# Kernel optimization log

Hardware: AMD Instinct MI355X
Metric: run time of the kernel (lower is better)

## Reference

```python
import jax, jax.numpy as jnp
import numpy as np

H, QK, VD = 16, 64, 64  # n_heads, qk_dim, v_dim

def _feature_map(t):
    # elu(x) + 1, the standard positive feature map for linear attention
    return jax.nn.elu(t) + 1.0

def setup_inputs() -> dict:
    key = jax.random.key(0)
    ks = jax.random.split(key, 5)
    B, T, D = 2, 4096, 1024
    s = 0.02
    return {
        "x": jax.random.normal(ks[0], (B, T, D), dtype=jnp.float32),
        "WQ": jax.random.normal(ks[1], (H * QK, D), dtype=jnp.float32) * s,
        "WK": jax.random.normal(ks[2], (H * QK, D), dtype=jnp.float32) * s,
        "WV": jax.random.normal(ks[3], (H * VD, D), dtype=jnp.float32) * s,
        "Wproj": jax.random.normal(ks[4], (D, VD), dtype=jnp.float32) * s,
        "start_pos": 0,
    }

def reference(x, WQ, WK, WV, Wproj, start_pos):
    B, T, D = x.shape
    # QKV projections (no bias), reshape to heads
    q = (x @ WQ.T).reshape(B, T, H, QK)
    k = (x @ WK.T).reshape(B, T, H, QK)
    v = (x @ WV.T).reshape(B, T, H, VD)
    q = _feature_map(q)
    k = _feature_map(k)
    # global key-value summary per head: [B,H,QK,VD]
    kv = jnp.einsum('bthd,bthm->bhdm', k, v)
    # normalizer: q . sum_t(k)
    z = 1.0 / jnp.einsum('bthd,bhd->bth', q, k.sum(axis=1))
    o = jnp.einsum('bthd,bhdm->bthm', q, kv) * z[..., None]  # [B,T,H,VD]
    # per-head output projection (module applies Linear(v_dim, dim) on last axis)
    return jnp.einsum('bthm,cm->bthc', o, Wproj)  # [B,T,H,D]
```

## Files before the change

kernel.cpp:

```cpp
#include <hip/hip_runtime.h>

#define Bb 2
#define Tt 4096
#define Dd 1024
#define Hh 16
#define QKd 64
#define VDd 64
#define BT (Bb*Tt)
#define NCH 16
#define CHUNK (Tt/NCH)

#define OFF_QF  0
#define OFF_KF  (OFF_QF + (size_t)BT*Dd)
#define OFF_V   (OFF_KF + (size_t)BT*512)
#define OFF_KVP (OFF_V + (size_t)BT*512)
#define OFF_KSP (OFF_KVP + (size_t)NCH*32*4096)
#define OFF_KV  (OFF_KSP + (size_t)NCH*32*64)
#define OFF_KS  (OFF_KV + (size_t)32*4096)
#define OFF_XA  (OFF_KS + (size_t)32*64)
#define OFF_WB  (OFF_XA + (size_t)BT*512)
#define OFF_KVQB (OFF_WB + (size_t)3072*512)
#define OFF_QSB (OFF_KVQB + (size_t)32*1024*32)

typedef __attribute__((ext_vector_type(8))) short short8;
typedef __attribute__((ext_vector_type(4))) float f32x4;

__device__ __forceinline__ float featmap(float x) {
    return x > 0.f ? x + 1.f : __expf(x);
}

__device__ __forceinline__ unsigned short bf16_rne(float f) {
    unsigned int u = __float_as_uint(f);
    unsigned int r = u + 0x7fffu + ((u >> 16) & 1u);
    return (unsigned short)(r >> 16);
}
__device__ __forceinline__ float bf16_to_f(unsigned short h) {
    return __uint_as_float(((unsigned int)h) << 16);
}

__global__ __launch_bounds__(256) void cast_a(const float* __restrict__ src,
                                              unsigned short* __restrict__ dst)
{
    int idx = blockIdx.x * 256 + threadIdx.x;
    int m = idx >> 8;
    int c = (idx & 255) << 2;
    float4 v = *(const float4*)&src[(size_t)m * 1024 + c];
    ushort4 o;
    o.x = bf16_rne(v.x); o.y = bf16_rne(v.y); o.z = bf16_rne(v.z); o.w = bf16_rne(v.w);
    *(ushort4*)&dst[(size_t)m * 1024 + c] = o;
}

__global__ __launch_bounds__(256) void cast_w3(const float* __restrict__ WQ,
                                               const float* __restrict__ WK,
                                               const float* __restrict__ WV,
                                               unsigned short* __restrict__ dst)
{
    int idx = blockIdx.x * 256 + threadIdx.x;
    int w = idx >> 18;
    int r = idx & 262143;
    const float* src = (w == 0) ? WQ : ((w == 1) ? WK : WV);
    int m = r >> 8;
    int c = (r & 255) << 2;
    float4 v = *(const float4*)&src[(size_t)m * 1024 + c];
    ushort4 o;
    o.x = bf16_rne(v.x); o.y = bf16_rne(v.y); o.z = bf16_rne(v.z); o.w = bf16_rne(v.w);
    *(ushort4*)&dst[(size_t)(w*1024 + m) * 1024 + c] = o;
}

#define GLLDS(gp, lp) __builtin_amdgcn_global_load_lds( \
    (const __attribute__((address_space(1))) void*)(gp), \
    (__attribute__((address_space(3))) void*)(lp), 16, 0, 0)

__global__ __launch_bounds__(512, 2) void gemm_qkv(const unsigned short* __restrict__ A,
                                                   const unsigned short* __restrict__ W,
                                                   float* __restrict__ qf,
                                                   unsigned short* __restrict__ kfb,
                                                   unsigned short* __restrict__ vfb)
{
    extern __shared__ unsigned short lds[];
    const int tid  = threadIdx.x;
    const int lane = tid & 63;
    const int wave = tid >> 6;
    const int wm = (wave >> 2) * 128;
    const int wn = (wave & 3) * 64;
    const int bid = blockIdx.x;
    const int nb = (bid & 7) * 48 + (bid >> 3);
    const int mblk = nb / 12, nblk = nb % 12;
    const int m0 = mblk * 256, n0 = nblk * 256;

    f32x4 acc[8][4] = {};

    auto stage = [&](int buf, int kt) {
        const int k0 = kt * 64;
        unsigned short* ab = &lds[buf * 32768];
        unsigned short* bb = ab + 16384;
        #pragma unroll
        for (int i = 0; i < 4; ++i) {
            int s = i * 512 + tid;
            int row = s >> 3, g = s & 7;
            int gl = g ^ (row & 7);
            GLLDS(&A[(size_t)(m0 + row) * 1024 + k0 + gl * 8], &ab[s * 8]);
        }
        #pragma unroll
        for (int i = 0; i < 4; ++i) {
            int s = i * 512 + tid;
            int row = s >> 3, g = s & 7;
            int gl = g ^ (row & 7);
            GLLDS(&W[(size_t)(n0 + row) * 1024 + k0 + gl * 8], &bb[s * 8]);
        }
    };

    stage(0, 0);
    for (int kt = 0; kt < 16; ++kt) {
        const int buf = kt & 1;
        if (kt + 1 < 16) {
            stage(buf ^ 1, kt + 1);
            asm volatile("s_waitcnt vmcnt(8)" ::: "memory");
        } else {
            asm volatile("s_waitcnt vmcnt(0)" ::: "memory");
        }
        __builtin_amdgcn_s_barrier();
        __builtin_amdgcn_sched_barrier(0);
        const unsigned short* ab = &lds[buf * 32768];
        const unsigned short* bb = ab + 16384;
        #pragma unroll
        for (int ks = 0; ks < 2; ++ks) {
            short8 af[8], bf2[4];
            #pragma unroll
            for (int mi = 0; mi < 8; ++mi) {
                int row = wm + mi * 16 + (lane & 15);
                int g = ks * 4 + (lane >> 4);
                af[mi] = *(const short8*)&ab[row * 64 + (g ^ (row & 7)) * 8];
            }
            #pragma unroll
            for (int ni = 0; ni < 4; ++ni) {
                int row = wn + ni * 16 + (lane & 15);
                int g = ks * 4 + (lane >> 4);
                bf2[ni] = *(const short8*)&bb[row * 64 + (g ^ (row & 7)) * 8];
            }
            __builtin_amdgcn_s_setprio(1);
            #pragma unroll
            for (int mi = 0; mi < 8; ++mi)
                #pragma unroll
                for (int ni = 0; ni < 4; ++ni)
                    acc[mi][ni] = __builtin_amdgcn_mfma_f32_16x16x32_bf16(af[mi], bf2[ni], acc[mi][ni], 0, 0, 0);
            __builtin_amdgcn_s_setprio(0);
        }
        __builtin_amdgcn_s_barrier();
        __builtin_amdgcn_sched_barrier(0);
    }

    const int c0 = n0 & 1023;
    if (n0 < 1024) {
        #pragma unroll
        for (int mi = 0; mi < 8; ++mi)
            #pragma unroll
            for (int ni = 0; ni < 4; ++ni)
                #pragma unroll
                for (int r = 0; r < 4; ++r) {
                    int row = m0 + wm + mi*16 + ((lane >> 4) << 2) + r;
                    int col = c0 + wn + ni*16 + (lane & 15);
                    qf[(size_t)row * 1024 + col] = featmap(acc[mi][ni][r]);
                }
    } else if (n0 < 2048) {
        #pragma unroll
        for (int mi = 0; mi < 8; ++mi)
            #pragma unroll
            for (int ni = 0; ni < 4; ++ni)
                #pragma unroll
                for (int r = 0; r < 4; ++r) {
                    int row = m0 + wm + mi*16 + ((lane >> 4) << 2) + r;
                    int col = c0 + wn + ni*16 + (lane & 15);
                    kfb[(size_t)row * 1024 + col] = bf16_rne(featmap(acc[mi][ni][r]));
                }
    } else {
        #pragma unroll
        for (int mi = 0; mi < 8; ++mi)
            #pragma unroll
            for (int ni = 0; ni < 4; ++ni)
                #pragma unroll
                for (int r = 0; r < 4; ++r) {
                    int row = m0 + wm + mi*16 + ((lane >> 4) << 2) + r;
                    int col = c0 + wn + ni*16 + (lane & 15);
                    vfb[(size_t)row * 1024 + col] = bf16_rne(acc[mi][ni][r]);
                }
    }
}

__global__ __launch_bounds__(256) void kv_partial(const unsigned short* __restrict__ kfb,
        const unsigned short* __restrict__ vfb, float* __restrict__ kvpart,
        float* __restrict__ kspart)
{
    const int bh = blockIdx.x;
    const int ch = blockIdx.y;
    const int b = bh >> 4, h = bh & 15;
    __shared__ float sk[8][64];
    __shared__ float sv[8][64];
    const int tid = threadIdx.x;
    const int r0 = (tid >> 4) << 2;
    const int c0 = (tid & 15) << 2;
    const int tt = tid >> 5;
    const int rem = tid & 31;
    const int which = rem >> 4;
    const int d4 = (rem & 15) << 2;
    const unsigned short* src = which ? vfb : kfb;
    float acc[4][4] = {};
    float ksl = 0.f;
    for (int t0 = ch * CHUNK; t0 < (ch + 1) * CHUNK; t0 += 8) {
        const int t = t0 + tt;
        ushort4 val = *(const ushort4*)&src[(size_t)(b*Tt + t)*Dd + h*QKd + d4];
        float4 f;
        f.x = bf16_to_f(val.x); f.y = bf16_to_f(val.y);
        f.z = bf16_to_f(val.z); f.w = bf16_to_f(val.w);
        __syncthreads();
        if (which) *(float4*)&sv[tt][d4] = f;
        else       *(float4*)&sk[tt][d4] = f;
        __syncthreads();
        #pragma unroll
        for (int s = 0; s < 8; ++s) {
            float4 k4v = *(const float4*)&sk[s][r0];
            float4 v4v = *(const float4*)&sv[s][c0];
            float kvv[4] = {k4v.x,k4v.y,k4v.z,k4v.w};
            float vvv[4] = {v4v.x,v4v.y,v4v.z,v4v.w};
            #pragma unroll
            for (int i = 0; i < 4; ++i)
                #pragma unroll
                for (int j = 0; j < 4; ++j)
                    acc[i][j] = fmaf(kvv[i], vvv[j], acc[i][j]);
        }
        if (tid < 64) {
            #pragma unroll
            for (int s = 0; s < 8; ++s) ksl += sk[s][tid];
        }
    }
    const size_t base = (size_t)(ch*32 + bh) * 4096;
    #pragma unroll
    for (int i = 0; i < 4; ++i) {
        float4 o = {acc[i][0], acc[i][1], acc[i][2], acc[i][3]};
        *(float4*)&kvpart[base + (r0+i)*64 + c0] = o;
    }
    if (tid < 64) kspart[(size_t)(ch*32 + bh)*64 + tid] = ksl;
}

__global__ __launch_bounds__(256) void kv_reduce(const float* __restrict__ kvpart,
        const float* __restrict__ kspart, float* __restrict__ kv, float* __restrict__ ksum)
{
    int g = blockIdx.x * 256 + threadIdx.x;
    if (g < 32*4096) {
        float s = 0.f;
        #pragma unroll
        for (int c = 0; c < NCH; ++c) s += kvpart[(size_t)c*(32*4096) + g];
        kv[g] = s;
    } else if (g < 32*4096 + 32*64) {
        int g2 = g - 32*4096;
        float s = 0.f;
        #pragma unroll
        for (int c = 0; c < NCH; ++c) s += kspart[(size_t)c*(32*64) + g2];
        ksum[g2] = s;
    }
}

__global__ __launch_bounds__(256) void kvpb_kernel(const float* __restrict__ kv,
        const float* __restrict__ wproj, unsigned short* __restrict__ kvqb)
{
    int flat = blockIdx.x * 256 + threadIdx.x;
    int d = flat & 63;
    int c = (flat >> 6) & 1023;
    int bh = flat >> 16;
    const float4* kr = (const float4*)&kv[(size_t)(bh*64 + d)*64];
    const float4* wr = (const float4*)&wproj[(size_t)c*64];
    float s = 0.f;
    #pragma unroll
    for (int m = 0; m < 16; ++m) {
        float4 a = kr[m], bq = wr[m];
        s += a.x*bq.x + a.y*bq.y + a.z*bq.z + a.w*bq.w;
    }
    kvqb[((size_t)bh*1024 + c) * 64 + d] = bf16_rne(s);
}

__global__ __launch_bounds__(256) void zq_kernel(const float* __restrict__ qf,
        const float* __restrict__ ksum, unsigned short* __restrict__ qsb)
{
    int row = blockIdx.x * 16 + (threadIdx.x >> 4);
    int l16 = threadIdx.x & 15;
    int bt = row >> 4, h = row & 15;
    int b = bt >> 12, t = bt & 4095;
    float4 qv = *(const float4*)&qf[(size_t)bt*1024 + h*64 + l16*4];
    float4 kq = *(const float4*)&ksum[(size_t)(b*16 + h)*64 + l16*4];
    float p = qv.x*kq.x + qv.y*kq.y + qv.z*kq.z + qv.w*kq.w;
    p += __shfl_xor(p, 1); p += __shfl_xor(p, 2);
    p += __shfl_xor(p, 4); p += __shfl_xor(p, 8);
    float zv = 1.f / p;
    ushort4 o;
    o.x = bf16_rne(qv.x*zv); o.y = bf16_rne(qv.y*zv);
    o.z = bf16_rne(qv.z*zv); o.w = bf16_rne(qv.w*zv);
    *(ushort4*)&qsb[(((size_t)(b*16 + h)*4096 + t) << 6) + l16*4] = o;
}

__global__ __launch_bounds__(256) void fgemm(const unsigned short* __restrict__ qsb,
        const unsigned short* __restrict__ kvqb, float* __restrict__ out)
{
    __shared__ unsigned short Als[2][128*32];
    __shared__ unsigned short Bls[2][128*32];
    const int tid  = threadIdx.x;
    const int lane = tid & 63;
    const int wave = tid >> 6;
    const int bh = blockIdx.z;
    const int b = bh >> 4, h = bh & 15;
    const int t0 = blockIdx.y * 128;
    const int c0 = blockIdx.x * 128;
    const int wr = (wave >> 1) * 64;
    const int wc = (wave & 1) * 64;
    f32x4 acc[4][4] = {};

    auto stage = [&](int buf, int kt) {
        const int k0 = kt * 32;
        #pragma unroll
        for (int i = 0; i < 2; ++i) {
            int s = i * 256 + tid;
            int row = s >> 2, g = s & 3;
            GLLDS(&qsb[((size_t)bh*4096 + t0 + row) * 64 + k0 + g * 8], &Als[buf][s * 8]);
            GLLDS(&kvqb[((size_t)bh*1024 + c0 + row) * 64 + k0 + g * 8], &Bls[buf][s * 8]);
        }
    };

    stage(0, 0);
    const int arow = (lane & 15) * 32 + (lane >> 4) * 8;
    for (int kt = 0; kt < 2; ++kt) {
        const int buf = kt & 1;
        __syncthreads();
        if (kt + 1 < 2) stage(buf ^ 1, kt + 1);
        short8 af[4], bfr[4];
        #pragma unroll
        for (int m = 0; m < 4; ++m)
            af[m] = *(const short8*)&Als[buf][(wr + m*16)*32 + arow];
        #pragma unroll
        for (int n = 0; n < 4; ++n)
            bfr[n] = *(const short8*)&Bls[buf][(wc + n*16)*32 + arow];
        #pragma unroll
        for (int m = 0; m < 4; ++m)
            #pragma unroll
            for (int n = 0; n < 4; ++n)
                acc[m][n] = __builtin_amdgcn_mfma_f32_16x16x32_bf16(af[m], bfr[n], acc[m][n], 0, 0, 0);
    }

    #pragma unroll
    for (int m = 0; m < 4; ++m) {
        #pragma unroll
        for (int n = 0; n < 4; ++n) {
            #pragma unroll
            for (int r = 0; r < 4; ++r) {
                int trow = t0 + wr + m*16 + ((lane >> 4) << 2) + r;
                int col = c0 + wc + n*16 + (lane & 15);
                out[((size_t)(b*4096 + trow)*16 + h)*1024 + col] = acc[m][n][r];
            }
        }
    }
}

extern "C" void kernel_launch(void* const* d_in, const int* in_sizes, int n_in,
                              void* d_out, int out_size, void* d_ws, size_t ws_size,
                              hipStream_t stream)
{
    const float* x  = (const float*)d_in[0];
    const float* WQ = (const float*)d_in[1];
    const float* WK = (const float*)d_in[2];
    const float* WV = (const float*)d_in[3];
    const float* Wp = (const float*)d_in[4];
    float* ws = (float*)d_ws;
    float* qf     = ws + OFF_QF;
    unsigned short* kfb = (unsigned short*)(ws + OFF_KF);
    unsigned short* vfb = (unsigned short*)(ws + OFF_V);
    float* kvpart = ws + OFF_KVP;
    float* kspart = ws + OFF_KSP;
    float* kv     = ws + OFF_KV;
    float* ksum   = ws + OFF_KS;
    unsigned short* xa   = (unsigned short*)(ws + OFF_XA);
    unsigned short* wb   = (unsigned short*)(ws + OFF_WB);
    unsigned short* kvqb = (unsigned short*)(ws + OFF_KVQB);
    unsigned short* qsb  = (unsigned short*)(ws + OFF_QSB);
    float* out = (float*)d_out;

    (void)hipFuncSetAttribute((const void*)gemm_qkv,
                              hipFuncAttributeMaxDynamicSharedMemorySize, 131072);

    dim3 blk(256);
    cast_a<<<(BT*1024/4)/256, blk, 0, stream>>>(x, xa);
    cast_w3<<<(3*1024*1024/4)/256, blk, 0, stream>>>(WQ, WK, WV, wb);
    gemm_qkv<<<384, 512, 131072, stream>>>(xa, wb, qf, kfb, vfb);
    kv_partial<<<dim3(32, NCH), blk, 0, stream>>>(kfb, vfb, kvpart, kspart);
    kv_reduce<<<(32*4096 + 32*64 + 255)/256, blk, 0, stream>>>(kvpart, kspart, kv, ksum);
    kvpb_kernel<<<(32*1024*64)/256, blk, 0, stream>>>(kv, Wp, kvqb);
    zq_kernel<<<(BT*Hh)/16, blk, 0, stream>>>(qf, ksum, qsb);
    fgemm<<<dim3(8, 32, 32), blk, 0, stream>>>(qsb, kvqb, out);
}
```

Before: 315.6 us.

## Merge cast kernels and restage kv_partial with larger time tiles

Fuses the two bf16 cast kernels into one launch, removing one kernel launch and its tail. Restructures kv_partial to stage 32 timesteps per iteration with padded LDS rows and wider per-thread loads, cutting the number of barriers per chunk. Halves the number of time chunks, which gives fewer blocks (256) but longer per-block loops and less partial-reduction data. The lower chunk count may reduce parallelism in kv_partial.

```diff
diff --git a/kernel.cpp b/kernel.cpp
--- a/kernel.cpp
+++ b/kernel.cpp
@@ -7,7 +7,7 @@
 #define QKd 64
 #define VDd 64
 #define BT (Bb*Tt)
-#define NCH 16
+#define NCH 8
 #define CHUNK (Tt/NCH)
 
 #define OFF_QF  0
@@ -38,33 +38,33 @@
     return __uint_as_float(((unsigned int)h) << 16);
 }
 
-__global__ __launch_bounds__(256) void cast_a(const float* __restrict__ src,
-                                              unsigned short* __restrict__ dst)
+__global__ __launch_bounds__(256) void cast_all(const float* __restrict__ x,
+                                                const float* __restrict__ WQ,
+                                                const float* __restrict__ WK,
+                                                const float* __restrict__ WV,
+                                                unsigned short* __restrict__ xa,
+                                                unsigned short* __restrict__ wbuf)
 {
     int idx = blockIdx.x * 256 + threadIdx.x;
-    int m = idx >> 8;
-    int c = (idx & 255) << 2;
-    float4 v = *(const float4*)&src[(size_t)m * 1024 + c];
-    ushort4 o;
-    o.x = bf16_rne(v.x); o.y = bf16_rne(v.y); o.z = bf16_rne(v.z); o.w = bf16_rne(v.w);
-    *(ushort4*)&dst[(size_t)m * 1024 + c] = o;
-}
-
-__global__ __launch_bounds__(256) void cast_w3(const float* __restrict__ WQ,
-                                               const float* __restrict__ WK,
-                                               const float* __restrict__ WV,
-                                               unsigned short* __restrict__ dst)
-{
-    int idx = blockIdx.x * 256 + threadIdx.x;
-    int w = idx >> 18;
-    int r = idx & 262143;
-    const float* src = (w == 0) ? WQ : ((w == 1) ? WK : WV);
-    int m = r >> 8;
-    int c = (r & 255) << 2;
-    float4 v = *(const float4*)&src[(size_t)m * 1024 + c];
-    ushort4 o;
-    o.x = bf16_rne(v.x); o.y = bf16_rne(v.y); o.z = bf16_rne(v.z); o.w = bf16_rne(v.w);
-    *(ushort4*)&dst[(size_t)(w*1024 + m) * 1024 + c] = o;
+    if (idx < 2097152) {
+        int m = idx >> 8;
+        int c = (idx & 255) << 2;
+        float4 v = *(const float4*)&x[(size_t)m * 1024 + c];
+        ushort4 o;
+        o.x = bf16_rne(v.x); o.y = bf16_rne(v.y); o.z = bf16_rne(v.z); o.w = bf16_rne(v.w);
+        *(ushort4*)&xa[(size_t)m * 1024 + c] = o;
+    } else {
+        int r = idx - 2097152;
+        int w = r >> 18;
+        int rr = r & 262143;
+        const float* src = (w == 0) ? WQ : ((w == 1) ? WK : WV);
+        int m = rr >> 8;
+        int c = (rr & 255) << 2;
+        float4 v = *(const float4*)&src[(size_t)m * 1024 + c];
+        ushort4 o;
+        o.x = bf16_rne(v.x); o.y = bf16_rne(v.y); o.z = bf16_rne(v.z); o.w = bf16_rne(v.w);
+        *(ushort4*)&wbuf[(size_t)(w*1024 + m) * 1024 + c] = o;
+    }
 }
 
 #define GLLDS(gp, lp) __builtin_amdgcn_global_load_lds( \
@@ -194,30 +194,37 @@
     const int bh = blockIdx.x;
     const int ch = blockIdx.y;
     const int b = bh >> 4, h = bh & 15;
-    __shared__ float sk[8][64];
-    __shared__ float sv[8][64];
+    __shared__ float sk[32][68];
+    __shared__ float sv[32][68];
     const int tid = threadIdx.x;
     const int r0 = (tid >> 4) << 2;
     const int c0 = (tid & 15) << 2;
-    const int tt = tid >> 5;
-    const int rem = tid & 31;
-    const int which = rem >> 4;
-    const int d4 = (rem & 15) << 2;
+    const int which = tid >> 7;
+    const int rr = (tid & 127) >> 2;
+    const int d16 = (tid & 3) << 4;
     const unsigned short* src = which ? vfb : kfb;
     float acc[4][4] = {};
     float ksl = 0.f;
-    for (int t0 = ch * CHUNK; t0 < (ch + 1) * CHUNK; t0 += 8) {
-        const int t = t0 + tt;
-        ushort4 val = *(const ushort4*)&src[(size_t)(b*Tt + t)*Dd + h*QKd + d4];
-        float4 f;
-        f.x = bf16_to_f(val.x); f.y = bf16_to_f(val.y);
-        f.z = bf16_to_f(val.z); f.w = bf16_to_f(val.w);
+    for (int t0 = ch * CHUNK; t0 < (ch + 1) * CHUNK; t0 += 32) {
+        const int t = t0 + rr;
+        const unsigned short* sp = &src[(size_t)(b*Tt + t)*Dd + h*QKd + d16];
+        ushort4 ua = *(const ushort4*)&sp[0];
+        ushort4 ub = *(const ushort4*)&sp[4];
+        ushort4 uc = *(const ushort4*)&sp[8];
+        ushort4 ud = *(const ushort4*)&sp[12];
+        float4 f0 = {bf16_to_f(ua.x), bf16_to_f(ua.y), bf16_to_f(ua.z), bf16_to_f(ua.w)};
+        float4 f1 = {bf16_to_f(ub.x), bf16_to_f(ub.y), bf16_to_f(ub.z), bf16_to_f(ub.w)};
+        float4 f2 = {bf16_to_f(uc.x), bf16_to_f(uc.y), bf16_to_f(uc.z), bf16_to_f(uc.w)};
+        float4 f3 = {bf16_to_f(ud.x), bf16_to_f(ud.y), bf16_to_f(ud.z), bf16_to_f(ud.w)};
         __syncthreads();
-        if (which) *(float4*)&sv[tt][d4] = f;
-        else       *(float4*)&sk[tt][d4] = f;
+        float* dst = which ? &sv[rr][d16] : &sk[rr][d16];
+        *(float4*)&dst[0]  = f0;
+        *(float4*)&dst[4]  = f1;
+        *(float4*)&dst[8]  = f2;
+        *(float4*)&dst[12] = f3;
         __syncthreads();
-        #pragma unroll
-        for (int s = 0; s < 8; ++s) {
+        #pragma unroll 8
+        for (int s = 0; s < 32; ++s) {
             float4 k4v = *(const float4*)&sk[s][r0];
             float4 v4v = *(const float4*)&sv[s][c0];
             float kvv[4] = {k4v.x,k4v.y,k4v.z,k4v.w};
@@ -229,8 +236,8 @@
                     acc[i][j] = fmaf(kvv[i], vvv[j], acc[i][j]);
         }
         if (tid < 64) {
-            #pragma unroll
-            for (int s = 0; s < 8; ++s) ksl += sk[s][tid];
+            #pragma unroll 8
+            for (int s = 0; s < 32; ++s) ksl += sk[s][tid];
         }
     }
     const size_t base = (size_t)(ch*32 + bh) * 4096;
@@ -385,8 +392,7 @@
                               hipFuncAttributeMaxDynamicSharedMemorySize, 131072);
 
     dim3 blk(256);
-    cast_a<<<(BT*1024/4)/256, blk, 0, stream>>>(x, xa);
-    cast_w3<<<(3*1024*1024/4)/256, blk, 0, stream>>>(WQ, WK, WV, wb);
+    cast_all<<<(2097152 + 786432)/256, blk, 0, stream>>>(x, WQ, WK, WV, xa, wb);
     gemm_qkv<<<384, 512, 131072, stream>>>(xa, wb, qf, kfb, vfb);
     kv_partial<<<dim3(32, NCH), blk, 0, stream>>>(kfb, vfb, kvpart, kspart);
     kv_reduce<<<(32*4096 + 32*64 + 255)/256, blk, 0, stream>>>(kvpart, kspart, kv, ksum);
```

New measurement: 318.3 us. Within noise of the previous version (+0.8%).
